# Optimization experiments

Measured on AMD Instinct MI355X. Metric: run time of the kernel, lower is better.

The kernel has to match this reference:

```python
import jax, jax.numpy as jnp
import numpy as np
import math

B, S, D, H, HD, W, G = 2, 4096, 768, 12, 64, 256, 64  # batch, seq, embed, heads, head_dim, one-sided window, n global tokens


def _chunk_keys(k, w):
    # k: [B,S,H,HD] -> overlapping 3w-wide key windows per w-sized query chunk: [B,nc,3w,H,HD]
    Bz, S_, Hh, HDd = k.shape
    nc = S_ // w
    kp = jnp.pad(k, ((0, 0), (w, w), (0, 0), (0, 0)))
    kb = kp.reshape(Bz, nc + 2, w, Hh, HDd)
    return jnp.concatenate([kb[:, 0:nc], kb[:, 1:nc + 1], kb[:, 2:nc + 2]], axis=2)


def _band_qk(q, k, w):
    # banded scores: out[b,i,h,j] = q_i . k_{i+j-w}, j in [0, 2w]
    Bz, S_, Hh, HDd = q.shape
    nc = S_ // w
    qc = q.reshape(Bz, nc, w, Hh, HDd)
    kc = _chunk_keys(k, w)
    sc = jnp.einsum('bcphd,bckhd->bchpk', qc, kc)  # [B,nc,H,w,3w]
    rows = jnp.arange(w)[:, None]
    cols = rows + jnp.arange(2 * w + 1)[None, :]   # within-window key index = p + j
    band = sc[:, :, :, rows, cols]                 # [B,nc,H,w,2w+1]
    return band.transpose(0, 1, 3, 2, 4).reshape(Bz, S_, Hh, 2 * w + 1)


def _band_pv(p, v, w):
    # out[b,i,h,:] = sum_j p[b,i,h,j] * v[b, i+j-w, h, :]
    Bz, S_, Hh, K = p.shape
    HDd = v.shape[-1]
    nc = S_ // w
    pc = p.reshape(Bz, nc, w, Hh, K).transpose(0, 1, 3, 2, 4)  # [B,nc,H,w,2w+1]
    rows = jnp.arange(w)[:, None]
    cols = rows + jnp.arange(2 * w + 1)[None, :]
    full = jnp.zeros((Bz, nc, Hh, w, 3 * w), p.dtype).at[:, :, :, rows, cols].set(pc)
    vc = _chunk_keys(v, w)
    out = jnp.einsum('bchpk,bckhd->bcphd', full, vc)  # [B,nc,w,H,HD]
    return out.reshape(Bz, S_, Hh, HDd)


def setup_inputs() -> dict:
    key = jax.random.key(0)
    ks = jax.random.split(key, 4)
    std = 0.02
    # attention mask: +1 = global (first G tokens), 0 = local windowed, no padding
    attention_mask = jnp.concatenate(
        [jnp.ones((B, G), jnp.int32), jnp.zeros((B, S - G), jnp.int32)], axis=1)
    return {
        'hidden_states': jax.random.normal(ks[0], (B, S, D), jnp.float32),
        'attention_mask': attention_mask,
        'Wq': jax.random.normal(ks[1], (D, D), jnp.float32) * std,
        'bq': jnp.zeros((D,), jnp.float32),
        'Wk': jax.random.normal(ks[2], (D, D), jnp.float32) * std,
        'bk': jnp.zeros((D,), jnp.float32),
        'Wv': jax.random.normal(ks[3], (D, D), jnp.float32) * std,
        'bv': jnp.zeros((D,), jnp.float32),
    }


def reference(hidden_states, attention_mask, Wq, bq, Wk, bk, Wv, bv):
    Bz, S_, D_ = hidden_states.shape
    HDd = D_ // H
    q = ((hidden_states @ Wq.T + bq) / math.sqrt(HDd)).reshape(Bz, S_, H, HDd)
    k = (hidden_states @ Wk.T + bk).reshape(Bz, S_, H, HDd)
    v = (hidden_states @ Wv.T + bv).reshape(Bz, S_, H, HDd)

    band = _band_qk(q, k, W)  # [B,S,H,2W+1]

    i = jnp.arange(S_)
    key_abs = i[:, None] + jnp.arange(2 * W + 1)[None, :] - W  # [S,2W+1]
    valid = (key_abs >= 0) & (key_abs < S_)
    kac = jnp.clip(key_abs, 0, S_ - 1)
    is_glob = attention_mask != 0                       # [B,S]
    glob_at_key = is_glob[:, kac] & valid[None]          # [B,S,2W+1]
    # remove global keys from windowed attention: d_mask = -10000 * head_dim (ones @ float_mask)
    band = band + jnp.where(glob_at_key, jnp.float32(-10000.0 * HDd), jnp.float32(0.0))[:, :, None, :]
    # mask_invalid_locations: out-of-range diagonals -> -inf
    band = jnp.where(valid[None, :, None, :], band, -jnp.inf)

    # global-token attention (first G tokens are the global ones)
    gs = jnp.einsum('bihd,bghd->bihg', q, k[:, :G])      # [B,S,H,G]

    scores = jnp.concatenate([gs, band], axis=-1)        # [B,S,H,G+2W+1]
    probs = jax.nn.softmax(scores.astype(jnp.float32), axis=-1)

    attn = jnp.einsum('bihg,bghd->bihd', probs[..., :G], v[:, :G]) + _band_pv(probs[..., G:], v, W)
    # [B,S,H,HD] -> (seq_len, bsz, embed_dim) as in the torch module
    return jnp.transpose(attn, (1, 0, 2, 3)).reshape(S_, Bz, D_)
```

## Files before the change

### kernel.cpp

```cpp
#include <hip/hip_runtime.h>
#include <hip/hip_bf16.h>
#include <stdint.h>

typedef __attribute__((ext_vector_type(4))) float          f32x4;
typedef __attribute__((ext_vector_type(4))) float          f4;
typedef __attribute__((ext_vector_type(2))) unsigned int   u32x2;
typedef __bf16 bf16_t;
typedef __attribute__((ext_vector_type(8))) bf16_t         bf16x8;
typedef __attribute__((ext_vector_type(8))) unsigned short u16x8;
typedef __attribute__((ext_vector_type(4))) unsigned short u16x4;

#define NB 2
#define NS 4096
#define ND 768
#define NH 12
#define NW 256

__device__ __forceinline__ unsigned short f2bf(float f) {
  union { float f; unsigned u; } v; v.f = f;
  unsigned r = v.u + 0x7fffu + ((v.u >> 16) & 1u);
  return (unsigned short)(r >> 16);
}

__device__ __forceinline__ unsigned pack2bf(float a, float b) {
  return (unsigned)f2bf(a) | ((unsigned)f2bf(b) << 16);
}

__device__ __forceinline__ void gload16(const void* g, void* l) {
  __builtin_amdgcn_global_load_lds((const __attribute__((address_space(1))) void*)g,
                                   (__attribute__((address_space(3))) void*)l, 16, 0, 0);
}

__global__ void cast_kernel(const float* __restrict__ in, unsigned short* __restrict__ out, int n4) {
  int i = blockIdx.x * blockDim.x + threadIdx.x;
  int stride = gridDim.x * blockDim.x;
  for (; i < n4; i += stride) {
    f4 v = reinterpret_cast<const f4*>(in)[i];
    u32x2 o = {pack2bf(v.x, v.y), pack2bf(v.z, v.w)};
    reinterpret_cast<u32x2*>(out)[i] = o;
  }
}

__global__ void cast3_kernel(const float* __restrict__ w0, const float* __restrict__ w1,
                             const float* __restrict__ w2, unsigned short* __restrict__ o0,
                             unsigned short* __restrict__ o1, unsigned short* __restrict__ o2) {
  const int n4 = 768 * 768 / 4;
  int i = blockIdx.x * blockDim.x + threadIdx.x;
  int stride = gridDim.x * blockDim.x;
  for (; i < 3 * n4; i += stride) {
    int m = i / n4, j = i - m * n4;
    const float* in = (m == 0) ? w0 : ((m == 1) ? w1 : w2);
    unsigned short* out = (m == 0) ? o0 : ((m == 1) ? o1 : o2);
    f4 v = reinterpret_cast<const f4*>(in)[j];
    u32x2 o = {pack2bf(v.x, v.y), pack2bf(v.z, v.w)};
    reinterpret_cast<u32x2*>(out)[j] = o;
  }
}

__global__ __launch_bounds__(256) void qkv_gemm(
    const unsigned short* __restrict__ Ab,
    const unsigned short* __restrict__ Wqb,
    const unsigned short* __restrict__ Wkb,
    const unsigned short* __restrict__ Wvb,
    const float* __restrict__ bqp, const float* __restrict__ bkp, const float* __restrict__ bvp,
    unsigned short* __restrict__ Qw, unsigned short* __restrict__ Kw, unsigned short* __restrict__ Vw) {
  __shared__ unsigned short As[128 * 32];
  __shared__ unsigned short Bs[128 * 32];

  int phys = blockIdx.x;
  int logical = (phys & 7) * 144 + (phys >> 3);
  int bn = logical % 18, bm = logical / 18;
  int mat = bn / 6, bnn = bn % 6;
  const unsigned short* Wm = (mat == 0) ? Wqb : ((mat == 1) ? Wkb : Wvb);
  const float* bias = (mat == 0) ? bqp : ((mat == 1) ? bkp : bvp);
  unsigned short* dst = (mat == 0) ? Qw : ((mat == 1) ? Kw : Vw);

  int t = threadIdx.x;
  int w = t >> 6, l = t & 63;
  int lg = l >> 4, ln = l & 15;
  int wm = w & 1, wn = w >> 1;

  f32x4 acc[4][4];
#pragma unroll
  for (int i = 0; i < 4; i++)
#pragma unroll
    for (int j = 0; j < 4; j++) acc[i][j] = f32x4{0.f, 0.f, 0.f, 0.f};

  for (int kt = 0; kt < 24; ++kt) {
    __syncthreads();
#pragma unroll
    for (int is = 0; is < 2; ++is) {
      int chunk = is * 256 + t;
      int row = chunk >> 2;
      int c8 = (chunk & 3) * 8;
      gload16(Ab + ((size_t)(bm * 128 + row)) * 768 + kt * 32 + c8, As + chunk * 8);
      gload16(Wm + ((size_t)(bnn * 128 + row)) * 768 + kt * 32 + c8, Bs + chunk * 8);
    }
    __syncthreads();
    bf16x8 af[4], bfr[4];
#pragma unroll
    for (int i = 0; i < 4; i++) {
      af[i]  = *reinterpret_cast<const bf16x8*>(As + (wm * 64 + i * 16 + ln) * 32 + lg * 8);
      bfr[i] = *reinterpret_cast<const bf16x8*>(Bs + (wn * 64 + i * 16 + ln) * 32 + lg * 8);
    }
#pragma unroll
    for (int i = 0; i < 4; i++)
#pragma unroll
      for (int j = 0; j < 4; j++)
        acc[i][j] = __builtin_amdgcn_mfma_f32_16x16x32_bf16(af[i], bfr[j], acc[i][j], 0, 0, 0);
  }

#pragma unroll
  for (int j = 0; j < 4; j++) {
    int col = bnn * 128 + wn * 64 + j * 16 + ln;
    float bv_ = bias[col];
    int hh = col >> 6, dd = col & 63;
#pragma unroll
    for (int i = 0; i < 4; i++) {
#pragma unroll
      for (int r = 0; r < 4; r++) {
        int tok = bm * 128 + wm * 64 + i * 16 + lg * 4 + r;
        int bb = tok >> 12, ss = tok & 4095;
        float v = acc[i][j][r] + bv_;
        if (mat == 0) v *= 0.1803368801111244f;
        dst[(((size_t)bb * 12 + hh) * 4096 + ss) * 64 + dd] = f2bf(v);
      }
    }
  }
}

__global__ __launch_bounds__(512) void attn_kernel(
    const unsigned short* __restrict__ Qw,
    const unsigned short* __restrict__ Kw,
    const unsigned short* __restrict__ Vw,
    const int* __restrict__ amask,
    float* __restrict__ out) {
  __shared__ unsigned short Ks[2][64 * 64];
  __shared__ unsigned short Vt[2][64 * 64];
  __shared__ unsigned Msk[128];

  int phys = blockIdx.x;
  int logical = (phys & 7) * 96 + (phys >> 3);
  int qc = logical & 31;
  int bh = logical >> 5;
  int b = bh / 12;
  int hh = bh % 12;
  int qbase = qc * 128;

  int t = threadIdx.x, w = t >> 6, l = t & 63;
  int lg = l >> 4, ln = l & 15;

  const unsigned short* Qbh = Qw + (size_t)bh * (NS * 64);
  const unsigned short* Kbh = Kw + (size_t)bh * (NS * 64);
  const unsigned short* Vbh = Vw + (size_t)bh * (NS * 64);
  const int* mrow = amask + b * NS;

#pragma unroll
  for (int r8 = 0; r8 < 8; ++r8) {
    int wp = r8 * 8 + w;
    unsigned long long bal = __ballot(mrow[wp * 64 + l] != 0);
    if (l == 0) {
      Msk[wp * 2] = (unsigned)bal;
      Msk[wp * 2 + 1] = (unsigned)(bal >> 32);
    }
  }

  int q = qbase + w * 16 + ln;
  int qwmin = qbase + w * 16;

  bf16x8 qf[2];
  {
    const unsigned short* qp = Qbh + (size_t)q * 64 + lg * 8;
    qf[0] = *reinterpret_cast<const bf16x8*>(qp);
    qf[1] = *reinterpret_cast<const bf16x8*>(qp + 32);
  }

  float m_s = -1e30f, l_s = 0.f;
  f32x4 oacc[4];
#pragma unroll
  for (int i = 0; i < 4; i++) oacc[i] = f32x4{0.f, 0.f, 0.f, 0.f};

  int tt_lo = (qbase >= 256) ? 0 : ((256 - qbase) >> 6);
  int tt_hi_raw = (NS + 192 - qbase) >> 6;
  int tt_hi = tt_hi_raw < 9 ? tt_hi_raw : 9;
  int ntl = tt_hi - tt_lo + 2;

  int krow = t >> 3, gran = t & 7;
  int p2 = t & 31, d0v = (t >> 5) * 4;

  {
    gload16(Kbh + (size_t)krow * 64 + (gran ^ (krow & 7)) * 8, &Ks[0][0] + t * 8);
    const unsigned short* vp0 = Vbh + (size_t)(2 * p2) * 64 + d0v;
    u16x4 va = *reinterpret_cast<const u16x4*>(vp0);
    u16x4 vb = *reinterpret_cast<const u16x4*>(vp0 + 64);
#pragma unroll
    for (int j = 0; j < 4; ++j) {
      int d = d0v + j;
      unsigned val = (unsigned)va[j] | ((unsigned)vb[j] << 16);
      *reinterpret_cast<unsigned*>(&Vt[0][0] + d * 64 + ((2 * p2) ^ ((d & 15) << 2))) = val;
    }
  }
  __syncthreads();

  for (int idx = 0; idx < ntl; ++idx) {
    int cur = idx & 1;
    int key0 = (idx == 0) ? 0 : (qbase - 256 + (tt_lo + idx - 1) * 64);
    bool has_next = (idx + 1) < ntl;

    u16x4 va, vb;
    if (has_next) {
      int nk0 = qbase - 256 + (tt_lo + idx) * 64;
      gload16(Kbh + (size_t)(nk0 + krow) * 64 + (gran ^ (krow & 7)) * 8,
              &Ks[cur ^ 1][0] + t * 8);
      const unsigned short* vp0 = Vbh + (size_t)(nk0 + 2 * p2) * 64 + d0v;
      va = *reinterpret_cast<const u16x4*>(vp0);
      vb = *reinterpret_cast<const u16x4*>(vp0 + 64);
    }

    bool relevant = (idx == 0) ||
                    ((key0 + 63 >= qwmin - 256) && (key0 <= qwmin + 15 + 256));
    if (relevant) {
      const unsigned short* ksb = &Ks[cur][0];
      f32x4 sa[4];
#pragma unroll
      for (int nt = 0; nt < 4; nt++) sa[nt] = f32x4{0.f, 0.f, 0.f, 0.f};
#pragma unroll
      for (int nt = 0; nt < 4; nt++) {
        int key = nt * 16 + ln;
#pragma unroll
        for (int ks = 0; ks < 2; ++ks) {
          int dby = (ks * 64 + lg * 16) ^ ((key & 7) << 4);
          bf16x8 kf = *reinterpret_cast<const bf16x8*>(ksb + key * 64 + (dby >> 1));
          sa[nt] = __builtin_amdgcn_mfma_f32_16x16x32_bf16(kf, qf[ks], sa[nt], 0, 0, 0);
        }
      }

      if (idx > 0) {
        unsigned mw0 = Msk[key0 >> 5], mw1 = Msk[(key0 >> 5) + 1];
        bool clean = ((mw0 | mw1) == 0) && (key0 >= qwmin - 241) && (key0 <= qwmin + 193);
        if (!clean) {
#pragma unroll
          for (int nt = 0; nt < 4; nt++) {
            unsigned mword = (nt & 2) ? mw1 : mw0;
#pragma unroll
            for (int r = 0; r < 4; r++) {
              int key = key0 + 16 * nt + 4 * lg + r;
              bool sup = (mword >> ((16 * (nt & 1) + 4 * lg + r) & 31)) & 1;
              bool bad = sup || ((unsigned)(key - q + NW) > 2u * NW);
              if (bad) sa[nt][r] = -1e30f;
            }
          }
        }
      }

      float tmax = sa[0][0];
#pragma unroll
      for (int nt = 0; nt < 4; nt++)
#pragma unroll
        for (int r = 0; r < 4; r++) tmax = fmaxf(tmax, sa[nt][r]);
      if (!__all(tmax - m_s <= 8.f)) {
        tmax = fmaxf(tmax, __shfl_xor(tmax, 16, 64));
        tmax = fmaxf(tmax, __shfl_xor(tmax, 32, 64));
        float mn = fmaxf(m_s, tmax);
        float scl = exp2f(m_s - mn);
        m_s = mn;
        l_s *= scl;
#pragma unroll
        for (int i = 0; i < 4; i++) oacc[i] *= scl;
      }
#pragma unroll
      for (int nt = 0; nt < 4; nt++)
#pragma unroll
        for (int r = 0; r < 4; r++) {
          float p = exp2f(sa[nt][r] - m_s);
          sa[nt][r] = p;
          l_s += p;
        }

      unsigned pk[4][2];
#pragma unroll
      for (int nt = 0; nt < 4; nt++) {
        pk[nt][0] = pack2bf(sa[nt][0], sa[nt][1]);
        pk[nt][1] = pack2bf(sa[nt][2], sa[nt][3]);
      }

      const unsigned short* vtb = &Vt[cur][0];
#pragma unroll
      for (int ks = 0; ks < 2; ++ks) {
        union { unsigned u[4]; bf16x8 v; } pf;
        pf.u[0] = pk[2 * ks][0];
        pf.u[1] = pk[2 * ks][1];
        pf.u[2] = pk[2 * ks + 1][0];
        pf.u[3] = pk[2 * ks + 1][1];
#pragma unroll
        for (int nt = 0; nt < 4; ++nt) {
          int d = nt * 16 + ln;
          int sw = (d & 15) << 2;
          int e0 = (32 * ks + 4 * lg) ^ sw;
          int e1 = (32 * ks + 16 + 4 * lg) ^ sw;
          union { u16x4 h[2]; bf16x8 v; } vf;
          vf.h[0] = *reinterpret_cast<const u16x4*>(vtb + d * 64 + e0);
          vf.h[1] = *reinterpret_cast<const u16x4*>(vtb + d * 64 + e1);
          oacc[nt] = __builtin_amdgcn_mfma_f32_16x16x32_bf16(vf.v, pf.v, oacc[nt], 0, 0, 0);
        }
      }
    }

    if (has_next) {
      unsigned short* vtn = &Vt[cur ^ 1][0];
#pragma unroll
      for (int j = 0; j < 4; ++j) {
        int d = d0v + j;
        unsigned val = (unsigned)va[j] | ((unsigned)vb[j] << 16);
        *reinterpret_cast<unsigned*>(vtn + d * 64 + ((2 * p2) ^ ((d & 15) << 2))) = val;
      }
    }
    __syncthreads();
  }

  l_s += __shfl_xor(l_s, 16, 64);
  l_s += __shfl_xor(l_s, 32, 64);
  float inv = 1.0f / l_s;
  float* orow = out + ((size_t)q * NB + b) * ND + hh * 64;
#pragma unroll
  for (int nt = 0; nt < 4; nt++) {
    f4 o;
#pragma unroll
    for (int r = 0; r < 4; r++) o[r] = oacc[nt][r] * inv;
    *reinterpret_cast<f4*>(orow + nt * 16 + 4 * lg) = o;
  }
}

extern "C" void kernel_launch(void* const* d_in, const int* in_sizes, int n_in,
                              void* d_out, int out_size, void* d_ws, size_t ws_size,
                              hipStream_t stream) {
  (void)in_sizes; (void)n_in; (void)out_size; (void)ws_size;
  const float* hidden = (const float*)d_in[0];
  const int*   amask  = (const int*)d_in[1];
  const float* Wq = (const float*)d_in[2];
  const float* bq = (const float*)d_in[3];
  const float* Wk = (const float*)d_in[4];
  const float* bk = (const float*)d_in[5];
  const float* Wv = (const float*)d_in[6];
  const float* bv = (const float*)d_in[7];
  float* out = (float*)d_out;

  char* p = (char*)d_ws;
  unsigned short* hb  = (unsigned short*)p; p += (size_t)8192 * 768 * 2;
  unsigned short* wqb = (unsigned short*)p; p += (size_t)768 * 768 * 2;
  unsigned short* wkb = (unsigned short*)p; p += (size_t)768 * 768 * 2;
  unsigned short* wvb = (unsigned short*)p; p += (size_t)768 * 768 * 2;
  unsigned short* Qws = (unsigned short*)p; p += (size_t)24 * 4096 * 64 * 2;
  unsigned short* Kws = (unsigned short*)p; p += (size_t)24 * 4096 * 64 * 2;
  unsigned short* Vws = (unsigned short*)p; p += (size_t)24 * 4096 * 64 * 2;

  cast_kernel<<<1024, 256, 0, stream>>>(hidden, hb, 8192 * 768 / 4);
  cast3_kernel<<<432, 256, 0, stream>>>(Wq, Wk, Wv, wqb, wkb, wvb);
  qkv_gemm<<<64 * 18, 256, 0, stream>>>(hb, wqb, wkb, wvb, bq, bk, bv, Qws, Kws, Vws);
  attn_kernel<<<24 * 32, 512, 0, stream>>>(Qws, Kws, Vws, amask, out);
}
```

Baseline: 196.5 us.

## Double-buffer QKV GEMM loads, stage epilogue via LDS, use fast exp and bf16 casts

```diff
diff --git a/kernel.cpp b/kernel.cpp
--- a/kernel.cpp
+++ b/kernel.cpp
@@ -24,6 +24,12 @@
 
 __device__ __forceinline__ unsigned pack2bf(float a, float b) {
   return (unsigned)f2bf(a) | ((unsigned)f2bf(b) << 16);
+}
+
+__device__ __forceinline__ float exp2_fast(float x) {
+  float r;
+  asm("v_exp_f32 %0, %1" : "=v"(r) : "v"(x));
+  return r;
 }
 
 __device__ __forceinline__ void gload16(const void* g, void* l) {
@@ -64,8 +70,7 @@
     const unsigned short* __restrict__ Wvb,
     const float* __restrict__ bqp, const float* __restrict__ bkp, const float* __restrict__ bvp,
     unsigned short* __restrict__ Qw, unsigned short* __restrict__ Kw, unsigned short* __restrict__ Vw) {
-  __shared__ unsigned short As[128 * 32];
-  __shared__ unsigned short Bs[128 * 32];
+  __shared__ unsigned short smem[2][2][128 * 32];
 
   int phys = blockIdx.x;
   int logical = (phys & 7) * 144 + (phys >> 3);
@@ -86,45 +91,73 @@
 #pragma unroll
     for (int j = 0; j < 4; j++) acc[i][j] = f32x4{0.f, 0.f, 0.f, 0.f};
 
+#pragma unroll
+  for (int is = 0; is < 2; ++is) {
+    int chunk = is * 256 + t;
+    int row = chunk >> 2;
+    int c8 = (chunk & 3) * 8;
+    gload16(Ab + ((size_t)(bm * 128 + row)) * 768 + c8, &smem[0][0][chunk * 8]);
+    gload16(Wm + ((size_t)(bnn * 128 + row)) * 768 + c8, &smem[0][1][chunk * 8]);
+  }
+  __syncthreads();
+
   for (int kt = 0; kt < 24; ++kt) {
-    __syncthreads();
-#pragma unroll
-    for (int is = 0; is < 2; ++is) {
-      int chunk = is * 256 + t;
-      int row = chunk >> 2;
-      int c8 = (chunk & 3) * 8;
-      gload16(Ab + ((size_t)(bm * 128 + row)) * 768 + kt * 32 + c8, As + chunk * 8);
-      gload16(Wm + ((size_t)(bnn * 128 + row)) * 768 + kt * 32 + c8, Bs + chunk * 8);
-    }
-    __syncthreads();
+    int cur = kt & 1;
+    if (kt < 23) {
+#pragma unroll
+      for (int is = 0; is < 2; ++is) {
+        int chunk = is * 256 + t;
+        int row = chunk >> 2;
+        int c8 = (chunk & 3) * 8;
+        gload16(Ab + ((size_t)(bm * 128 + row)) * 768 + (kt + 1) * 32 + c8,
+                &smem[cur ^ 1][0][chunk * 8]);
+        gload16(Wm + ((size_t)(bnn * 128 + row)) * 768 + (kt + 1) * 32 + c8,
+                &smem[cur ^ 1][1][chunk * 8]);
+      }
+    }
     bf16x8 af[4], bfr[4];
 #pragma unroll
     for (int i = 0; i < 4; i++) {
-      af[i]  = *reinterpret_cast<const bf16x8*>(As + (wm * 64 + i * 16 + ln) * 32 + lg * 8);
-      bfr[i] = *reinterpret_cast<const bf16x8*>(Bs + (wn * 64 + i * 16 + ln) * 32 + lg * 8);
+      af[i]  = *reinterpret_cast<const bf16x8*>(&smem[cur][0][(wm * 64 + i * 16 + ln) * 32 + lg * 8]);
+      bfr[i] = *reinterpret_cast<const bf16x8*>(&smem[cur][1][(wn * 64 + i * 16 + ln) * 32 + lg * 8]);
     }
 #pragma unroll
     for (int i = 0; i < 4; i++)
 #pragma unroll
       for (int j = 0; j < 4; j++)
         acc[i][j] = __builtin_amdgcn_mfma_f32_16x16x32_bf16(af[i], bfr[j], acc[i][j], 0, 0, 0);
-  }
-
+    __syncthreads();
+  }
+
+  unsigned short* ep = &smem[0][0][0];
 #pragma unroll
   for (int j = 0; j < 4; j++) {
-    int col = bnn * 128 + wn * 64 + j * 16 + ln;
-    float bv_ = bias[col];
-    int hh = col >> 6, dd = col & 63;
+    int col = wn * 64 + j * 16 + ln;
+    float bv_ = bias[bnn * 128 + col];
 #pragma unroll
     for (int i = 0; i < 4; i++) {
 #pragma unroll
       for (int r = 0; r < 4; r++) {
-        int tok = bm * 128 + wm * 64 + i * 16 + lg * 4 + r;
-        int bb = tok >> 12, ss = tok & 4095;
+        int row = wm * 64 + i * 16 + lg * 4 + r;
         float v = acc[i][j][r] + bv_;
         if (mat == 0) v *= 0.1803368801111244f;
-        dst[(((size_t)bb * 12 + hh) * 4096 + ss) * 64 + dd] = f2bf(v);
-      }
+        int g = col >> 3;
+        ep[row * 128 + (((g ^ (row & 15)) << 3) | (col & 7))] = f2bf(v);
+      }
+    }
+  }
+  __syncthreads();
+  {
+    int row = t >> 1, half = t & 1;
+    int tok = bm * 128 + row;
+    int bb = tok >> 12, ss = tok & 4095;
+    int head = bnn * 2 + half;
+    unsigned short* drow = dst + (((size_t)bb * 12 + head) * 4096 + ss) * 64;
+#pragma unroll
+    for (int kk8 = 0; kk8 < 8; ++kk8) {
+      int g = (half * 8 + kk8) ^ (row & 15);
+      *reinterpret_cast<u16x8*>(drow + kk8 * 8) =
+          *reinterpret_cast<const u16x8*>(ep + row * 128 + g * 8);
     }
   }
 }
@@ -262,7 +295,7 @@
         tmax = fmaxf(tmax, __shfl_xor(tmax, 16, 64));
         tmax = fmaxf(tmax, __shfl_xor(tmax, 32, 64));
         float mn = fmaxf(m_s, tmax);
-        float scl = exp2f(m_s - mn);
+        float scl = exp2_fast(m_s - mn);
         m_s = mn;
         l_s *= scl;
 #pragma unroll
@@ -272,26 +305,24 @@
       for (int nt = 0; nt < 4; nt++)
 #pragma unroll
         for (int r = 0; r < 4; r++) {
-          float p = exp2f(sa[nt][r] - m_s);
+          float p = exp2_fast(sa[nt][r] - m_s);
           sa[nt][r] = p;
           l_s += p;
         }
 
-      unsigned pk[4][2];
-#pragma unroll
-      for (int nt = 0; nt < 4; nt++) {
-        pk[nt][0] = pack2bf(sa[nt][0], sa[nt][1]);
-        pk[nt][1] = pack2bf(sa[nt][2], sa[nt][3]);
+      union { bf16_t bb[8]; bf16x8 v; } pf0, pf1;
+#pragma unroll
+      for (int r = 0; r < 4; r++) {
+        pf0.bb[r]     = (bf16_t)sa[0][r];
+        pf0.bb[4 + r] = (bf16_t)sa[1][r];
+        pf1.bb[r]     = (bf16_t)sa[2][r];
+        pf1.bb[4 + r] = (bf16_t)sa[3][r];
       }
 
       const unsigned short* vtb = &Vt[cur][0];
 #pragma unroll
       for (int ks = 0; ks < 2; ++ks) {
-        union { unsigned u[4]; bf16x8 v; } pf;
-        pf.u[0] = pk[2 * ks][0];
-        pf.u[1] = pk[2 * ks][1];
-        pf.u[2] = pk[2 * ks + 1][0];
-        pf.u[3] = pk[2 * ks + 1][1];
+        bf16x8 pv = ks ? pf1.v : pf0.v;
 #pragma unroll
         for (int nt = 0; nt < 4; ++nt) {
           int d = nt * 16 + ln;
@@ -301,7 +332,7 @@
           union { u16x4 h[2]; bf16x8 v; } vf;
           vf.h[0] = *reinterpret_cast<const u16x4*>(vtb + d * 64 + e0);
           vf.h[1] = *reinterpret_cast<const u16x4*>(vtb + d * 64 + e1);
-          oacc[nt] = __builtin_amdgcn_mfma_f32_16x16x32_bf16(vf.v, pf.v, oacc[nt], 0, 0, 0);
+          oacc[nt] = __builtin_amdgcn_mfma_f32_16x16x32_bf16(vf.v, pv, oacc[nt], 0, 0, 0);
         }
       }
     }
```

After: 193.0 us. Within noise of the previous version (-1.8%).
